# Kernel optimization log

Measured on AMD Instinct MI355X. Metric: run time of the kernel, lower is better.

Reference implementation:

```python
import jax, jax.numpy as jnp
import numpy as np

CONF_TH = 0.25   # default conf_thresh in non_max_suppression
NMS_TH = 0.35    # default nms_thresh


def setup_inputs() -> dict:
    key = jax.random.key(0)
    # [N, C=5+num_classes, H, W]
    preds = jax.random.normal(key, (64, 85, 32, 32), dtype=jnp.float32)
    return {"preds": preds}


def _decode(preds):
    """Faithful box decode: [N,C,H,W] -> [N, H*W, 6] (x1,y1,x2,y2,score,cls)."""
    N, C, H, W = preds.shape
    p = jnp.transpose(preds, (0, 2, 3, 1))           # [N,H,W,C]
    pobj = p[..., 0]
    preg = p[..., 1:5]
    pcls = p[..., 5:]
    score = pobj * jnp.max(pcls, axis=-1)             # obj * max-class
    cls = jax.lax.stop_gradient(jnp.argmax(pcls, axis=-1).astype(preds.dtype))
    gy, gx = jnp.meshgrid(jnp.arange(H, dtype=preds.dtype),
                          jnp.arange(W, dtype=preds.dtype), indexing="ij")
    bw = jax.nn.sigmoid(preg[..., 2])
    bh = jax.nn.sigmoid(preg[..., 3])
    bcx = (jnp.tanh(preg[..., 0]) + gx) / W
    bcy = (jnp.tanh(preg[..., 1]) + gy) / H
    x1 = bcx - 0.5 * bw
    y1 = bcy - 0.5 * bh
    x2 = bcx + 0.5 * bw
    y2 = bcy + 0.5 * bh
    bboxes = jnp.stack([x1, y1, x2, y2, score, cls], axis=-1)  # [N,H,W,6]
    return bboxes.reshape(N, H * W, 6)


def _iou_matrix(boxes):
    """[M,4] xyxy -> [M,M] pairwise IoU."""
    x1, y1, x2, y2 = boxes[:, 0], boxes[:, 1], boxes[:, 2], boxes[:, 3]
    area = (x2 - x1) * (y2 - y1)
    iw = jnp.clip(jnp.minimum(x2[:, None], x2[None, :]) - jnp.maximum(x1[:, None], x1[None, :]), 0.0)
    ih = jnp.clip(jnp.minimum(y2[:, None], y2[None, :]) - jnp.maximum(y1[:, None], y1[None, :]), 0.0)
    inter = iw * ih
    return inter / (area[:, None] + area[None, :] - inter + 1e-9)


def _nms_single(bb):
    """Greedy class-aware NMS on one image's [M,6] boxes.
    Equivalent to: filter score>CONF_TH then torchvision.batched_nms.
    Returns keep mask [M] in the original box order (fixed shape)."""
    M = bb.shape[0]
    order = jnp.argsort(-bb[:, 4])                    # descending score
    b = bb[order]
    iou = _iou_matrix(b[:, :4])
    same_cls = b[:, 5][:, None] == b[:, 5][None, :]
    supp_mat = (iou > NMS_TH) & same_cls              # [M,M]
    valid_s = b[:, 4] > CONF_TH

    def body(i, keep):
        suppressed = jnp.any(keep & supp_mat[i])
        return keep.at[i].set(valid_s[i] & ~suppressed)

    keep_s = jax.lax.fori_loop(0, M, body, jnp.zeros((M,), jnp.bool_))
    # scatter back to original order
    return jnp.zeros((M,), jnp.bool_).at[order].set(keep_s)


def reference(preds):
    bboxes = _decode(preds)                # [N, HW, 6]
    keep = jax.vmap(_nms_single)(bboxes)   # [N, HW] bool keep mask
    return bboxes, keep
```

## Files before the change

### kernel.cpp

```cpp
#include <hip/hip_runtime.h>
#include <math.h>

#define NIMG 64
#define HW   1024
#define NCH  85
#define NCLS 80
#define CONF_TH 0.25f
#define NMS_TH  0.35f

__device__ __forceinline__ float fast_tanh(float x) {
  float e = __expf(2.0f * x);
  return 1.0f - 2.0f * __builtin_amdgcn_rcpf(e + 1.0f);
}
__device__ __forceinline__ float fast_sigmoid(float x) {
  return __builtin_amdgcn_rcpf(1.0f + __expf(-x));
}

__global__ __launch_bounds__(256) void decode_kernel(const float* __restrict__ preds,
                                                     float* __restrict__ out) {
  int gid = blockIdx.x * 256 + threadIdx.x;
  int n = gid >> 10;
  int t = gid & 1023;
  const float* bp = preds + (size_t)n * (NCH * HW) + t;

  float pobj = bp[0];
  float tx = bp[(size_t)1 * HW];
  float ty = bp[(size_t)2 * HW];
  float tw = bp[(size_t)3 * HW];
  float th = bp[(size_t)4 * HW];

  float b0, b1, b2, b3;
  int i0, i1, i2, i3;
  b0 = bp[(size_t)(5 +  0) * HW]; i0 =  0;
  b1 = bp[(size_t)(5 + 20) * HW]; i1 = 20;
  b2 = bp[(size_t)(5 + 40) * HW]; i2 = 40;
  b3 = bp[(size_t)(5 + 60) * HW]; i3 = 60;
#pragma unroll
  for (int c = 1; c < 20; ++c) {
    float v0 = bp[(size_t)(5 +  0 + c) * HW];
    float v1 = bp[(size_t)(5 + 20 + c) * HW];
    float v2 = bp[(size_t)(5 + 40 + c) * HW];
    float v3 = bp[(size_t)(5 + 60 + c) * HW];
    if (v0 > b0) { b0 = v0; i0 =  0 + c; }
    if (v1 > b1) { b1 = v1; i1 = 20 + c; }
    if (v2 > b2) { b2 = v2; i2 = 40 + c; }
    if (v3 > b3) { b3 = v3; i3 = 60 + c; }
  }
  float best = b0; int bc = i0;
  if (b1 > best) { best = b1; bc = i1; }
  if (b2 > best) { best = b2; bc = i2; }
  if (b3 > best) { best = b3; bc = i3; }

  float score = pobj * best;

  float gx = (float)(t & 31);
  float gy = (float)(t >> 5);
  float bcx = (fast_tanh(tx) + gx) * 0.03125f;
  float bcy = (fast_tanh(ty) + gy) * 0.03125f;
  float bw = fast_sigmoid(tw);
  float bh = fast_sigmoid(th);

  float x1 = bcx - 0.5f * bw, y1 = bcy - 0.5f * bh;
  float x2 = bcx + 0.5f * bw, y2 = bcy + 0.5f * bh;

  float2* ob = (float2*)(out + (size_t)gid * 6);
  ob[0] = make_float2(x1, y1);
  ob[1] = make_float2(x2, y2);
  ob[2] = make_float2(score, (float)bc);
}

__global__ __launch_bounds__(1024) void nms_kernel(const float* __restrict__ boxes,
                                                   float* __restrict__ keepOut) {
  int n = blockIdx.x;
  int t = threadIdx.x;

  __shared__ float sx1[HW], sy1[HW], sx2[HW], sy2[HW], sarea[HW], sscore[HW];
  __shared__ int scls[HW];
  __shared__ int bucket[HW];
  __shared__ int sorted[HW];
  __shared__ int srank[HW];
  __shared__ unsigned long long supp[HW];
  __shared__ int cnt[NCLS], offs[NCLS], start[NCLS];

  if (t < NCLS) cnt[t] = 0;

  size_t gb = (size_t)n * HW + t;
  const float2* ib = (const float2*)(boxes + gb * 6);
  float2 a01 = ib[0];
  float2 a23 = ib[1];
  float2 a45 = ib[2];
  float x1 = a01.x, y1 = a01.y, x2 = a23.x, y2 = a23.y;
  float score = a45.x;
  int bc = (int)a45.y;

  float aar = (x2 - x1) * (y2 - y1);
  sx1[t] = x1; sy1[t] = y1; sx2[t] = x2; sy2[t] = y2;
  sarea[t] = aar;
  sscore[t] = score;
  scls[t] = bc;
  bool valid = score > CONF_TH;
  keepOut[gb] = 0.0f;
  __syncthreads();

  if (valid) atomicAdd(&cnt[bc], 1);
  __syncthreads();

  if (t < 64) {
    int c0 = (2 * t < NCLS) ? cnt[2 * t] : 0;
    int c1 = (2 * t + 1 < NCLS) ? cnt[2 * t + 1] : 0;
    int ps = c0 + c1;
    int x = ps;
#pragma unroll
    for (int d = 1; d < 64; d <<= 1) {
      int y = __shfl_up(x, d, 64);
      if (t >= d) x += y;
    }
    int excl = x - ps;
    if (2 * t < NCLS)     { start[2 * t] = excl;          offs[2 * t] = excl; }
    if (2 * t + 1 < NCLS) { start[2 * t + 1] = excl + c0; offs[2 * t + 1] = excl + c0; }
  }
  __syncthreads();

  if (valid) {
    int p = atomicAdd(&offs[bc], 1);
    bucket[p] = t;
  }
  __syncthreads();

  if (valid) {
    int s0 = start[bc], m = cnt[bc];
    int r = 0;
    for (int j = 0; j < m; ++j) {
      int jb = bucket[s0 + j];
      float sj = sscore[jb];
      r += (sj > score) || (sj == score && jb < t);
    }
    srank[t] = r;
    sorted[s0 + r] = t;
  }
  __syncthreads();

  if (valid) {
    int s0 = start[bc];
    int a = srank[t];
    int lim = a < 64 ? a : 64;
    unsigned long long mask = 0ull;
    for (int b = 0; b < lim; ++b) {
      int jb = sorted[s0 + b];
      float iw = fminf(x2, sx2[jb]) - fmaxf(x1, sx1[jb]);
      float ih = fminf(y2, sy2[jb]) - fmaxf(y1, sy1[jb]);
      iw = fmaxf(iw, 0.0f);
      ih = fmaxf(ih, 0.0f);
      float inter = iw * ih;
      float iou = inter / (aar + sarea[jb] - inter + 1e-9f);
      if (iou > NMS_TH) mask |= (1ull << b);
    }
    supp[s0 + a] = mask;
  }
  __syncthreads();

  if (t < NCLS) {
    int m = cnt[t], s0 = start[t];
    if (m <= 64) {
      unsigned long long kept = 0ull;
      for (int a = 0; a < m; ++a) {
        unsigned long long sa = supp[s0 + a];
        if ((sa & kept) == 0ull) {
          kept |= (1ull << a);
          keepOut[(size_t)n * HW + sorted[s0 + a]] = 1.0f;
        }
      }
    } else {
      for (int a = 0; a < m; ++a) {
        int ia = sorted[s0 + a];
        float ax1 = sx1[ia], ay1 = sy1[ia], ax2 = sx2[ia], ay2 = sy2[ia];
        float ar2 = sarea[ia];
        bool kp = true;
        for (int b = 0; b < a; ++b) {
          if (!bucket[s0 + b]) continue;
          int jb = sorted[s0 + b];
          float iw = fminf(ax2, sx2[jb]) - fmaxf(ax1, sx1[jb]);
          float ih = fminf(ay2, sy2[jb]) - fmaxf(ay1, sy1[jb]);
          iw = fmaxf(iw, 0.0f);
          ih = fmaxf(ih, 0.0f);
          float inter = iw * ih;
          float iou = inter / (ar2 + sarea[jb] - inter + 1e-9f);
          if (iou > NMS_TH) { kp = false; break; }
        }
        bucket[s0 + a] = kp ? 1 : 0;
        if (kp) keepOut[(size_t)n * HW + ia] = 1.0f;
      }
    }
  }
}

extern "C" void kernel_launch(void* const* d_in, const int* in_sizes, int n_in,
                              void* d_out, int out_size, void* d_ws, size_t ws_size,
                              hipStream_t stream) {
  const float* preds = (const float*)d_in[0];
  float* out = (float*)d_out;
  float* keepOut = out + (size_t)NIMG * HW * 6;

  decode_kernel<<<NIMG * HW / 256, 256, 0, stream>>>(preds, out);
  nms_kernel<<<NIMG, HW, 0, stream>>>(out, keepOut);
}
```

Before: 73.85 us.

## Split NMS per image into four class-quarter blocks of 256 threads

The NMS kernel now launches four 256-thread blocks per image, each handling a quarter of the classes (20). Each thread loads four boxes, and the keep-mask zeroing moves into the decode kernel. The aim is more blocks across the CUs and a shorter serial greedy phase per block. In exchange, every block reloads all 1024 boxes into shared memory, so that work is done four times per image.

```diff
diff --git a/kernel.cpp b/kernel.cpp
--- a/kernel.cpp
+++ b/kernel.cpp
@@ -5,6 +5,7 @@
 #define HW   1024
 #define NCH  85
 #define NCLS 80
+#define CQ   20
 #define CONF_TH 0.25f
 #define NMS_TH  0.35f
 
@@ -17,7 +18,8 @@
 }
 
 __global__ __launch_bounds__(256) void decode_kernel(const float* __restrict__ preds,
-                                                     float* __restrict__ out) {
+                                                     float* __restrict__ out,
+                                                     float* __restrict__ keepOut) {
   int gid = blockIdx.x * 256 + threadIdx.x;
   int n = gid >> 10;
   int t = gid & 1023;
@@ -67,99 +69,112 @@
   ob[0] = make_float2(x1, y1);
   ob[1] = make_float2(x2, y2);
   ob[2] = make_float2(score, (float)bc);
-}
-
-__global__ __launch_bounds__(1024) void nms_kernel(const float* __restrict__ boxes,
-                                                   float* __restrict__ keepOut) {
-  int n = blockIdx.x;
+
+  keepOut[gid] = 0.0f;
+}
+
+__global__ __launch_bounds__(256) void nms_kernel(const float* __restrict__ boxes,
+                                                  float* __restrict__ keepOut) {
+  int n  = blockIdx.x >> 2;
+  int c0 = (blockIdx.x & 3) * CQ;
   int t = threadIdx.x;
 
   __shared__ float sx1[HW], sy1[HW], sx2[HW], sy2[HW], sarea[HW], sscore[HW];
-  __shared__ int scls[HW];
   __shared__ int bucket[HW];
   __shared__ int sorted[HW];
-  __shared__ int srank[HW];
   __shared__ unsigned long long supp[HW];
-  __shared__ int cnt[NCLS], offs[NCLS], start[NCLS];
-
-  if (t < NCLS) cnt[t] = 0;
-
-  size_t gb = (size_t)n * HW + t;
-  const float2* ib = (const float2*)(boxes + gb * 6);
-  float2 a01 = ib[0];
-  float2 a23 = ib[1];
-  float2 a45 = ib[2];
-  float x1 = a01.x, y1 = a01.y, x2 = a23.x, y2 = a23.y;
-  float score = a45.x;
-  int bc = (int)a45.y;
-
-  float aar = (x2 - x1) * (y2 - y1);
-  sx1[t] = x1; sy1[t] = y1; sx2[t] = x2; sy2[t] = y2;
-  sarea[t] = aar;
-  sscore[t] = score;
-  scls[t] = bc;
-  bool valid = score > CONF_TH;
-  keepOut[gb] = 0.0f;
-  __syncthreads();
-
-  if (valid) atomicAdd(&cnt[bc], 1);
+  __shared__ int cnt[CQ], offs[CQ], start[CQ];
+
+  if (t < CQ) cnt[t] = 0;
+
+  float px1[4], py1[4], px2[4], py2[4], par[4], psc[4];
+  int pcl[4]; bool pval[4];
+#pragma unroll
+  for (int k = 0; k < 4; ++k) {
+    int p = t + 256 * k;
+    const float2* ib = (const float2*)(boxes + ((size_t)n * HW + p) * 6);
+    float2 a01 = ib[0];
+    float2 a23 = ib[1];
+    float2 a45 = ib[2];
+    px1[k] = a01.x; py1[k] = a01.y; px2[k] = a23.x; py2[k] = a23.y;
+    psc[k] = a45.x;
+    int cl = (int)a45.y;
+    pcl[k] = cl;
+    par[k] = (px2[k] - px1[k]) * (py2[k] - py1[k]);
+    sx1[p] = px1[k]; sy1[p] = py1[k]; sx2[p] = px2[k]; sy2[p] = py2[k];
+    sarea[p] = par[k];
+    sscore[p] = psc[k];
+    pval[k] = (psc[k] > CONF_TH) && (cl >= c0) && (cl < c0 + CQ);
+  }
+  __syncthreads();
+
+#pragma unroll
+  for (int k = 0; k < 4; ++k)
+    if (pval[k]) atomicAdd(&cnt[pcl[k] - c0], 1);
   __syncthreads();
 
   if (t < 64) {
-    int c0 = (2 * t < NCLS) ? cnt[2 * t] : 0;
-    int c1 = (2 * t + 1 < NCLS) ? cnt[2 * t + 1] : 0;
-    int ps = c0 + c1;
-    int x = ps;
-#pragma unroll
-    for (int d = 1; d < 64; d <<= 1) {
+    int c = (t < CQ) ? cnt[t] : 0;
+    int x = c;
+#pragma unroll
+    for (int d = 1; d < 32; d <<= 1) {
       int y = __shfl_up(x, d, 64);
       if (t >= d) x += y;
     }
-    int excl = x - ps;
-    if (2 * t < NCLS)     { start[2 * t] = excl;          offs[2 * t] = excl; }
-    if (2 * t + 1 < NCLS) { start[2 * t + 1] = excl + c0; offs[2 * t + 1] = excl + c0; }
-  }
-  __syncthreads();
-
-  if (valid) {
-    int p = atomicAdd(&offs[bc], 1);
-    bucket[p] = t;
-  }
-  __syncthreads();
-
-  if (valid) {
-    int s0 = start[bc], m = cnt[bc];
-    int r = 0;
-    for (int j = 0; j < m; ++j) {
-      int jb = bucket[s0 + j];
-      float sj = sscore[jb];
-      r += (sj > score) || (sj == score && jb < t);
-    }
-    srank[t] = r;
-    sorted[s0 + r] = t;
-  }
-  __syncthreads();
-
-  if (valid) {
-    int s0 = start[bc];
-    int a = srank[t];
-    int lim = a < 64 ? a : 64;
-    unsigned long long mask = 0ull;
-    for (int b = 0; b < lim; ++b) {
-      int jb = sorted[s0 + b];
-      float iw = fminf(x2, sx2[jb]) - fmaxf(x1, sx1[jb]);
-      float ih = fminf(y2, sy2[jb]) - fmaxf(y1, sy1[jb]);
-      iw = fmaxf(iw, 0.0f);
-      ih = fmaxf(ih, 0.0f);
-      float inter = iw * ih;
-      float iou = inter / (aar + sarea[jb] - inter + 1e-9f);
-      if (iou > NMS_TH) mask |= (1ull << b);
-    }
-    supp[s0 + a] = mask;
-  }
-  __syncthreads();
-
-  if (t < NCLS) {
+    if (t < CQ) { start[t] = x - c; offs[t] = x - c; }
+  }
+  __syncthreads();
+
+#pragma unroll
+  for (int k = 0; k < 4; ++k)
+    if (pval[k]) {
+      int p = atomicAdd(&offs[pcl[k] - c0], 1);
+      bucket[p] = t + 256 * k;
+    }
+  __syncthreads();
+
+  int rk[4];
+#pragma unroll
+  for (int k = 0; k < 4; ++k)
+    if (pval[k]) {
+      int p = t + 256 * k;
+      int cl = pcl[k] - c0;
+      int s0 = start[cl], m = cnt[cl];
+      float sc = psc[k];
+      int r = 0;
+      for (int j = 0; j < m; ++j) {
+        int jb = bucket[s0 + j];
+        float sj = sscore[jb];
+        r += (sj > sc) || (sj == sc && jb < p);
+      }
+      rk[k] = r;
+      sorted[s0 + r] = p;
+    }
+  __syncthreads();
+
+#pragma unroll
+  for (int k = 0; k < 4; ++k)
+    if (pval[k]) {
+      int cl = pcl[k] - c0;
+      int s0 = start[cl];
+      int a = rk[k];
+      int lim = a < 64 ? a : 64;
+      unsigned long long mask = 0ull;
+      for (int b = 0; b < lim; ++b) {
+        int jb = sorted[s0 + b];
+        float iw = fminf(px2[k], sx2[jb]) - fmaxf(px1[k], sx1[jb]);
+        float ih = fminf(py2[k], sy2[jb]) - fmaxf(py1[k], sy1[jb]);
+        iw = fmaxf(iw, 0.0f);
+        ih = fmaxf(ih, 0.0f);
+        float inter = iw * ih;
+        float iou = inter / (par[k] + sarea[jb] - inter + 1e-9f);
+        if (iou > NMS_TH) mask |= (1ull << b);
+      }
+      supp[s0 + a] = mask;
+    }
+  __syncthreads();
+
+  if (t < CQ) {
     int m = cnt[t], s0 = start[t];
     if (m <= 64) {
       unsigned long long kept = 0ull;
@@ -201,6 +216,6 @@
   float* out = (float*)d_out;
   float* keepOut = out + (size_t)NIMG * HW * 6;
 
-  decode_kernel<<<NIMG * HW / 256, 256, 0, stream>>>(preds, out);
-  nms_kernel<<<NIMG, HW, 0, stream>>>(out, keepOut);
-}
+  decode_kernel<<<NIMG * HW / 256, 256, 0, stream>>>(preds, out, keepOut);
+  nms_kernel<<<NIMG * 4, 256, 0, stream>>>(out, keepOut);
+}
```

Measured after the change: 86.31 us. +16.9%, slower.

## Fuse decode and NMS via last-block-per-image atomic counter

Applied to the files above, without the earlier changes.

Decode and NMS now run in one kernel of 256-thread blocks. Each block decodes its boxes, then bumps a per-image atomic counter, and the last of the four blocks for an image runs that image's NMS, with each thread handling four boxes. This removes the second kernel launch and the gap between kernels. In exchange NMS runs on 256 threads instead of 1024, each block reserves the full NMS shared memory, which can lower decode occupancy, and a memset is added to reset the counters. The old two-kernel path remains as a fallback when no workspace is available.

```diff
diff --git a/kernel.cpp b/kernel.cpp
--- a/kernel.cpp
+++ b/kernel.cpp
@@ -16,9 +16,12 @@
   return __builtin_amdgcn_rcpf(1.0f + __expf(-x));
 }
 
-__global__ __launch_bounds__(256) void decode_kernel(const float* __restrict__ preds,
-                                                     float* __restrict__ out) {
-  int gid = blockIdx.x * 256 + threadIdx.x;
+__global__ __launch_bounds__(256) void fused_kernel(const float* __restrict__ preds,
+                                                    float* __restrict__ out,
+                                                    float* __restrict__ keepOut,
+                                                    int* __restrict__ counters) {
+  int tid = threadIdx.x;
+  int gid = blockIdx.x * 256 + tid;
   int n = gid >> 10;
   int t = gid & 1023;
   const float* bp = preds + (size_t)n * (NCH * HW) + t;
@@ -67,100 +70,117 @@
   ob[0] = make_float2(x1, y1);
   ob[1] = make_float2(x2, y2);
   ob[2] = make_float2(score, (float)bc);
-}
-
-__global__ __launch_bounds__(1024) void nms_kernel(const float* __restrict__ boxes,
-                                                   float* __restrict__ keepOut) {
-  int n = blockIdx.x;
-  int t = threadIdx.x;
+
+  keepOut[gid] = 0.0f;
+
+  __shared__ int amLast;
+  __threadfence();
+  __syncthreads();
+  if (tid == 0) amLast = (atomicAdd(&counters[n], 1) == 3);
+  __syncthreads();
+  if (!amLast) return;
+  __threadfence();
 
   __shared__ float sx1[HW], sy1[HW], sx2[HW], sy2[HW], sarea[HW], sscore[HW];
-  __shared__ int scls[HW];
   __shared__ int bucket[HW];
   __shared__ int sorted[HW];
-  __shared__ int srank[HW];
   __shared__ unsigned long long supp[HW];
   __shared__ int cnt[NCLS], offs[NCLS], start[NCLS];
 
-  if (t < NCLS) cnt[t] = 0;
-
-  size_t gb = (size_t)n * HW + t;
-  const float2* ib = (const float2*)(boxes + gb * 6);
-  float2 a01 = ib[0];
-  float2 a23 = ib[1];
-  float2 a45 = ib[2];
-  float x1 = a01.x, y1 = a01.y, x2 = a23.x, y2 = a23.y;
-  float score = a45.x;
-  int bc = (int)a45.y;
-
-  float aar = (x2 - x1) * (y2 - y1);
-  sx1[t] = x1; sy1[t] = y1; sx2[t] = x2; sy2[t] = y2;
-  sarea[t] = aar;
-  sscore[t] = score;
-  scls[t] = bc;
-  bool valid = score > CONF_TH;
-  keepOut[gb] = 0.0f;
-  __syncthreads();
-
-  if (valid) atomicAdd(&cnt[bc], 1);
-  __syncthreads();
-
-  if (t < 64) {
-    int c0 = (2 * t < NCLS) ? cnt[2 * t] : 0;
-    int c1 = (2 * t + 1 < NCLS) ? cnt[2 * t + 1] : 0;
+  if (tid < NCLS) cnt[tid] = 0;
+
+  float px1[4], py1[4], px2[4], py2[4], par[4], psc[4];
+  int pcl[4]; bool pval[4];
+#pragma unroll
+  for (int k = 0; k < 4; ++k) {
+    int p = tid + 256 * k;
+    const float2* ib = (const float2*)(out + ((size_t)n * HW + p) * 6);
+    float2 a01 = ib[0];
+    float2 a23 = ib[1];
+    float2 a45 = ib[2];
+    px1[k] = a01.x; py1[k] = a01.y; px2[k] = a23.x; py2[k] = a23.y;
+    psc[k] = a45.x;
+    pcl[k] = (int)a45.y;
+    par[k] = (px2[k] - px1[k]) * (py2[k] - py1[k]);
+    sx1[p] = px1[k]; sy1[p] = py1[k]; sx2[p] = px2[k]; sy2[p] = py2[k];
+    sarea[p] = par[k];
+    sscore[p] = psc[k];
+    pval[k] = psc[k] > CONF_TH;
+  }
+  __syncthreads();
+
+#pragma unroll
+  for (int k = 0; k < 4; ++k)
+    if (pval[k]) atomicAdd(&cnt[pcl[k]], 1);
+  __syncthreads();
+
+  if (tid < 64) {
+    int c0 = (2 * tid < NCLS) ? cnt[2 * tid] : 0;
+    int c1 = (2 * tid + 1 < NCLS) ? cnt[2 * tid + 1] : 0;
     int ps = c0 + c1;
     int x = ps;
 #pragma unroll
     for (int d = 1; d < 64; d <<= 1) {
       int y = __shfl_up(x, d, 64);
-      if (t >= d) x += y;
+      if (tid >= d) x += y;
     }
     int excl = x - ps;
-    if (2 * t < NCLS)     { start[2 * t] = excl;          offs[2 * t] = excl; }
-    if (2 * t + 1 < NCLS) { start[2 * t + 1] = excl + c0; offs[2 * t + 1] = excl + c0; }
-  }
-  __syncthreads();
-
-  if (valid) {
-    int p = atomicAdd(&offs[bc], 1);
-    bucket[p] = t;
-  }
-  __syncthreads();
-
-  if (valid) {
-    int s0 = start[bc], m = cnt[bc];
-    int r = 0;
-    for (int j = 0; j < m; ++j) {
-      int jb = bucket[s0 + j];
-      float sj = sscore[jb];
-      r += (sj > score) || (sj == score && jb < t);
-    }
-    srank[t] = r;
-    sorted[s0 + r] = t;
-  }
-  __syncthreads();
-
-  if (valid) {
-    int s0 = start[bc];
-    int a = srank[t];
-    int lim = a < 64 ? a : 64;
-    unsigned long long mask = 0ull;
-    for (int b = 0; b < lim; ++b) {
-      int jb = sorted[s0 + b];
-      float iw = fminf(x2, sx2[jb]) - fmaxf(x1, sx1[jb]);
-      float ih = fminf(y2, sy2[jb]) - fmaxf(y1, sy1[jb]);
-      iw = fmaxf(iw, 0.0f);
-      ih = fmaxf(ih, 0.0f);
-      float inter = iw * ih;
-      float iou = inter / (aar + sarea[jb] - inter + 1e-9f);
-      if (iou > NMS_TH) mask |= (1ull << b);
-    }
-    supp[s0 + a] = mask;
-  }
-  __syncthreads();
-
-  if (t < NCLS) {
-    int m = cnt[t], s0 = start[t];
+    if (2 * tid < NCLS)     { start[2 * tid] = excl;          offs[2 * tid] = excl; }
+    if (2 * tid + 1 < NCLS) { start[2 * tid + 1] = excl + c0; offs[2 * tid + 1] = excl + c0; }
+  }
+  __syncthreads();
+
+#pragma unroll
+  for (int k = 0; k < 4; ++k)
+    if (pval[k]) {
+      int p = atomicAdd(&offs[pcl[k]], 1);
+      bucket[p] = tid + 256 * k;
+    }
+  __syncthreads();
+
+  int rk[4];
+#pragma unroll
+  for (int k = 0; k < 4; ++k)
+    if (pval[k]) {
+      int p = tid + 256 * k;
+      int cl = pcl[k];
+      int s0 = start[cl], m = cnt[cl];
+      float sc = psc[k];
+      int r = 0;
+      for (int j = 0; j < m; ++j) {
+        int jb = bucket[s0 + j];
+        float sj = sscore[jb];
+        r += (sj > sc) || (sj == sc && jb < p);
+      }
+      rk[k] = r;
+      sorted[s0 + r] = p;
+    }
+  __syncthreads();
+
+#pragma unroll
+  for (int k = 0; k < 4; ++k)
+    if (pval[k]) {
+      int cl = pcl[k];
+      int s0 = start[cl];
+      int a = rk[k];
+      int lim = a < 64 ? a : 64;
+      unsigned long long mask = 0ull;
+      for (int b = 0; b < lim; ++b) {
+        int jb = sorted[s0 + b];
+        float iw = fminf(px2[k], sx2[jb]) - fmaxf(px1[k], sx1[jb]);
+        float ih = fminf(py2[k], sy2[jb]) - fmaxf(py1[k], sy1[jb]);
+        iw = fmaxf(iw, 0.0f);
+        ih = fmaxf(ih, 0.0f);
+        float inter = iw * ih;
+        float iou = inter / (par[k] + sarea[jb] - inter + 1e-9f);
+        if (iou > NMS_TH) mask |= (1ull << b);
+      }
+      supp[s0 + a] = mask;
+    }
+  __syncthreads();
+
+  if (tid < NCLS) {
+    int m = cnt[tid], s0 = start[tid];
     if (m <= 64) {
       unsigned long long kept = 0ull;
       for (int a = 0; a < m; ++a) {
@@ -194,6 +214,184 @@
   }
 }
 
+__global__ __launch_bounds__(256) void decode_kernel(const float* __restrict__ preds,
+                                                     float* __restrict__ out,
+                                                     float* __restrict__ keepOut) {
+  int gid = blockIdx.x * 256 + threadIdx.x;
+  int n = gid >> 10;
+  int t = gid & 1023;
+  const float* bp = preds + (size_t)n * (NCH * HW) + t;
+
+  float pobj = bp[0];
+  float tx = bp[(size_t)1 * HW];
+  float ty = bp[(size_t)2 * HW];
+  float tw = bp[(size_t)3 * HW];
+  float th = bp[(size_t)4 * HW];
+
+  float b0, b1, b2, b3;
+  int i0, i1, i2, i3;
+  b0 = bp[(size_t)(5 +  0) * HW]; i0 =  0;
+  b1 = bp[(size_t)(5 + 20) * HW]; i1 = 20;
+  b2 = bp[(size_t)(5 + 40) * HW]; i2 = 40;
+  b3 = bp[(size_t)(5 + 60) * HW]; i3 = 60;
+#pragma unroll
+  for (int c = 1; c < 20; ++c) {
+    float v0 = bp[(size_t)(5 +  0 + c) * HW];
+    float v1 = bp[(size_t)(5 + 20 + c) * HW];
+    float v2 = bp[(size_t)(5 + 40 + c) * HW];
+    float v3 = bp[(size_t)(5 + 60 + c) * HW];
+    if (v0 > b0) { b0 = v0; i0 =  0 + c; }
+    if (v1 > b1) { b1 = v1; i1 = 20 + c; }
+    if (v2 > b2) { b2 = v2; i2 = 40 + c; }
+    if (v3 > b3) { b3 = v3; i3 = 60 + c; }
+  }
+  float best = b0; int bc = i0;
+  if (b1 > best) { best = b1; bc = i1; }
+  if (b2 > best) { best = b2; bc = i2; }
+  if (b3 > best) { best = b3; bc = i3; }
+
+  float score = pobj * best;
+
+  float gx = (float)(t & 31);
+  float gy = (float)(t >> 5);
+  float bcx = (fast_tanh(tx) + gx) * 0.03125f;
+  float bcy = (fast_tanh(ty) + gy) * 0.03125f;
+  float bw = fast_sigmoid(tw);
+  float bh = fast_sigmoid(th);
+
+  float x1 = bcx - 0.5f * bw, y1 = bcy - 0.5f * bh;
+  float x2 = bcx + 0.5f * bw, y2 = bcy + 0.5f * bh;
+
+  float2* ob = (float2*)(out + (size_t)gid * 6);
+  ob[0] = make_float2(x1, y1);
+  ob[1] = make_float2(x2, y2);
+  ob[2] = make_float2(score, (float)bc);
+
+  keepOut[gid] = 0.0f;
+}
+
+__global__ __launch_bounds__(1024) void nms_kernel(const float* __restrict__ boxes,
+                                                   float* __restrict__ keepOut) {
+  int n = blockIdx.x;
+  int t = threadIdx.x;
+
+  __shared__ float sx1[HW], sy1[HW], sx2[HW], sy2[HW], sarea[HW], sscore[HW];
+  __shared__ int bucket[HW];
+  __shared__ int sorted[HW];
+  __shared__ int srank[HW];
+  __shared__ unsigned long long supp[HW];
+  __shared__ int cnt[NCLS], offs[NCLS], start[NCLS];
+
+  if (t < NCLS) cnt[t] = 0;
+
+  size_t gb = (size_t)n * HW + t;
+  const float2* ib = (const float2*)(boxes + gb * 6);
+  float2 a01 = ib[0];
+  float2 a23 = ib[1];
+  float2 a45 = ib[2];
+  float x1 = a01.x, y1 = a01.y, x2 = a23.x, y2 = a23.y;
+  float score = a45.x;
+  int bc = (int)a45.y;
+
+  float aar = (x2 - x1) * (y2 - y1);
+  sx1[t] = x1; sy1[t] = y1; sx2[t] = x2; sy2[t] = y2;
+  sarea[t] = aar;
+  sscore[t] = score;
+  bool valid = score > CONF_TH;
+  __syncthreads();
+
+  if (valid) atomicAdd(&cnt[bc], 1);
+  __syncthreads();
+
+  if (t < 64) {
+    int c0 = (2 * t < NCLS) ? cnt[2 * t] : 0;
+    int c1 = (2 * t + 1 < NCLS) ? cnt[2 * t + 1] : 0;
+    int ps = c0 + c1;
+    int x = ps;
+#pragma unroll
+    for (int d = 1; d < 64; d <<= 1) {
+      int y = __shfl_up(x, d, 64);
+      if (t >= d) x += y;
+    }
+    int excl = x - ps;
+    if (2 * t < NCLS)     { start[2 * t] = excl;          offs[2 * t] = excl; }
+    if (2 * t + 1 < NCLS) { start[2 * t + 1] = excl + c0; offs[2 * t + 1] = excl + c0; }
+  }
+  __syncthreads();
+
+  if (valid) {
+    int p = atomicAdd(&offs[bc], 1);
+    bucket[p] = t;
+  }
+  __syncthreads();
+
+  if (valid) {
+    int s0 = start[bc], m = cnt[bc];
+    int r = 0;
+    for (int j = 0; j < m; ++j) {
+      int jb = bucket[s0 + j];
+      float sj = sscore[jb];
+      r += (sj > score) || (sj == score && jb < t);
+    }
+    srank[t] = r;
+    sorted[s0 + r] = t;
+  }
+  __syncthreads();
+
+  if (valid) {
+    int s0 = start[bc];
+    int a = srank[t];
+    int lim = a < 64 ? a : 64;
+    unsigned long long mask = 0ull;
+    for (int b = 0; b < lim; ++b) {
+      int jb = sorted[s0 + b];
+      float iw = fminf(x2, sx2[jb]) - fmaxf(x1, sx1[jb]);
+      float ih = fminf(y2, sy2[jb]) - fmaxf(y1, sy1[jb]);
+      iw = fmaxf(iw, 0.0f);
+      ih = fmaxf(ih, 0.0f);
+      float inter = iw * ih;
+      float iou = inter / (aar + sarea[jb] - inter + 1e-9f);
+      if (iou > NMS_TH) mask |= (1ull << b);
+    }
+    supp[s0 + a] = mask;
+  }
+  __syncthreads();
+
+  if (t < NCLS) {
+    int m = cnt[t], s0 = start[t];
+    if (m <= 64) {
+      unsigned long long kept = 0ull;
+      for (int a = 0; a < m; ++a) {
+        unsigned long long sa = supp[s0 + a];
+        if ((sa & kept) == 0ull) {
+          kept |= (1ull << a);
+          keepOut[(size_t)n * HW + sorted[s0 + a]] = 1.0f;
+        }
+      }
+    } else {
+      for (int a = 0; a < m; ++a) {
+        int ia = sorted[s0 + a];
+        float ax1 = sx1[ia], ay1 = sy1[ia], ax2 = sx2[ia], ay2 = sy2[ia];
+        float ar2 = sarea[ia];
+        bool kp = true;
+        for (int b = 0; b < a; ++b) {
+          if (!bucket[s0 + b]) continue;
+          int jb = sorted[s0 + b];
+          float iw = fminf(ax2, sx2[jb]) - fmaxf(ax1, sx1[jb]);
+          float ih = fminf(ay2, sy2[jb]) - fmaxf(ay1, sy1[jb]);
+          iw = fmaxf(iw, 0.0f);
+          ih = fmaxf(ih, 0.0f);
+          float inter = iw * ih;
+          float iou = inter / (ar2 + sarea[jb] - inter + 1e-9f);
+          if (iou > NMS_TH) { kp = false; break; }
+        }
+        bucket[s0 + a] = kp ? 1 : 0;
+        if (kp) keepOut[(size_t)n * HW + ia] = 1.0f;
+      }
+    }
+  }
+}
+
 extern "C" void kernel_launch(void* const* d_in, const int* in_sizes, int n_in,
                               void* d_out, int out_size, void* d_ws, size_t ws_size,
                               hipStream_t stream) {
@@ -201,6 +399,11 @@
   float* out = (float*)d_out;
   float* keepOut = out + (size_t)NIMG * HW * 6;
 
-  decode_kernel<<<NIMG * HW / 256, 256, 0, stream>>>(preds, out);
-  nms_kernel<<<NIMG, HW, 0, stream>>>(out, keepOut);
-}
+  if (d_ws != nullptr && ws_size >= NIMG * sizeof(int)) {
+    hipMemsetAsync(d_ws, 0, NIMG * sizeof(int), stream);
+    fused_kernel<<<NIMG * HW / 256, 256, 0, stream>>>(preds, out, keepOut, (int*)d_ws);
+  } else {
+    decode_kernel<<<NIMG * HW / 256, 256, 0, stream>>>(preds, out, keepOut);
+    nms_kernel<<<NIMG, HW, 0, stream>>>(out, keepOut);
+  }
+}
```

Result: slower. 124.1 us (+68.1%).
